# Kernel tuning notes

Hardware: AMD Instinct MI355X
Metric: run time of the kernel (lower is better)

## Reference

```python
import jax, jax.numpy as jnp
import numpy as np
from math import sqrt

NUM_HEADS = 16
NUM_KV_HEADS = 4
ROPE_BASE = 10000.0


def setup_inputs() -> dict:
    key = jax.random.key(0)
    ks = jax.random.split(key, 9)
    B, S, E = 4, 2048, 2048
    KV_DIM = NUM_KV_HEADS * (E // NUM_HEADS)  # 512
    s = 0.02
    return {
        "x": jax.random.normal(ks[0], (B, S, E), jnp.float32),
        "wq": jax.random.normal(ks[1], (E, E), jnp.float32) * s,
        "bq": jnp.zeros((E,), jnp.float32),
        "wk": jax.random.normal(ks[2], (KV_DIM, E), jnp.float32) * s,
        "bk": jnp.zeros((KV_DIM,), jnp.float32),
        "wv": jax.random.normal(ks[3], (KV_DIM, E), jnp.float32) * s,
        "bv": jnp.zeros((KV_DIM,), jnp.float32),
        "wo": jax.random.normal(ks[4], (E, E), jnp.float32) * s,
        "bo": jnp.zeros((E,), jnp.float32),
    }


def _rope_cos_sin(seq_len, head_dim, dtype):
    inv_freq = 1.0 / (ROPE_BASE ** (jnp.arange(0, head_dim, 2, dtype=jnp.float32) / head_dim))
    pos = jnp.arange(seq_len, dtype=jnp.float32)
    freqs = pos[:, None] * inv_freq[None, :]            # [S, D/2]
    emb = jnp.concatenate([freqs, freqs], axis=-1)      # [S, D]
    return jnp.cos(emb).astype(dtype), jnp.sin(emb).astype(dtype)


def _apply_rope(t, cos, sin):
    # t: [B, H, S, D]; cos/sin: [S, D]
    d2 = t.shape[-1] // 2
    rot = jnp.concatenate([-t[..., d2:], t[..., :d2]], axis=-1)
    return t * cos[None, None, :, :] + rot * sin[None, None, :, :]


def reference(x, wq, bq, wk, bk, wv, bv, wo, bo):
    B, S, E = x.shape
    H, KV = NUM_HEADS, NUM_KV_HEADS
    D = E // H
    G = H // KV

    q = (x @ wq.T + bq).reshape(B, S, H, D).transpose(0, 2, 1, 3)   # [B,H,S,D]
    k = (x @ wk.T + bk).reshape(B, S, KV, D).transpose(0, 2, 1, 3)  # [B,KV,S,D]
    v = (x @ wv.T + bv).reshape(B, S, KV, D).transpose(0, 2, 1, 3)

    cos, sin = _rope_cos_sin(S, D, x.dtype)
    q = _apply_rope(q, cos, sin)
    k = _apply_rope(k, cos, sin)

    # GQA: expand each kv head group_size times (contiguous repeat)
    k = jnp.repeat(k, G, axis=1)  # [B,H,S,D]
    v = jnp.repeat(v, G, axis=1)

    scores = jnp.einsum("bhqd,bhkd->bhqk", q, k)
    causal = jnp.triu(jnp.ones((S, S), dtype=bool), k=1)
    scores = jnp.where(causal[None, None, :, :], -jnp.inf, scores)
    attn = jax.nn.softmax(scores / sqrt(D), axis=-1)
    out = jnp.einsum("bhqk,bhkd->bhqd", attn, v)        # [B,H,S,D]
    out = out.transpose(0, 2, 1, 3).reshape(B, S, E)
    return out @ wo.T + bo
```

## Files before the change

### kernel.cpp

```cpp
#include <hip/hip_runtime.h>
#include <stdint.h>
#include <math.h>

typedef __attribute__((ext_vector_type(8))) short s16x8;
typedef __attribute__((ext_vector_type(4))) short s16x4;
typedef __attribute__((ext_vector_type(4))) float f32x4;

#define NEGH (-1.0e30f)

__device__ __forceinline__ short f2bf(float f) {
  union { float f; unsigned int i; } c; c.f = f;
  unsigned int lsb = (c.i >> 16) & 1u;
  c.i += 0x7fffu + lsb;
  return (short)(c.i >> 16);
}
__device__ __forceinline__ float bf2f(short u) {
  union { unsigned int i; float f; } c;
  c.i = ((unsigned int)(unsigned short)u) << 16;
  return c.f;
}

#define GLOAD_LDS16(gp, lp)                                                  \
  __builtin_amdgcn_global_load_lds(                                          \
      (__attribute__((address_space(1))) void*)(void*)(gp),                  \
      (__attribute__((address_space(3))) void*)(lp), 16, 0, 0)

__global__ __launch_bounds__(256) void cvt_kernel(const float* __restrict__ in,
                                                  short* __restrict__ out)
{
  const size_t i = ((size_t)blockIdx.x * 256 + threadIdx.x) * 4;
  const float4 v = *(const float4*)(in + i);
  s16x4 o = { f2bf(v.x), f2bf(v.y), f2bf(v.z), f2bf(v.w) };
  *(s16x4*)(out + i) = o;
}

__global__ __launch_bounds__(256) void gemm_bt(
    const short* __restrict__ A, const short* __restrict__ W,
    const float* __restrict__ bias, const float* __restrict__ bias2,
    void* __restrict__ C, void* __restrict__ C2,
    int M, int N, int K, int omode)
{
  __shared__ __align__(16) short As[128 * 64];
  __shared__ __align__(16) short Bs[128 * 64];

  const int t = threadIdx.x;
  const int l = t & 63;
  const int w = t >> 6;
  const int lane16 = l & 15;
  const int quad = l >> 4;
  const int wm = w >> 1, wn = w & 1;

  int bx = blockIdx.x, by = blockIdx.y;
  if (gridDim.x == 8 && gridDim.y == 64) {
    const int lid = blockIdx.x + 8 * blockIdx.y;
    const int xcd = lid & 7, idx = lid >> 3;
    by = xcd * 8 + (idx >> 3);
    bx = idx & 7;
  }
  const int mb0 = by * 128;
  const int nb0 = bx * 128;

  const f32x4 zero = {0.f, 0.f, 0.f, 0.f};
  f32x4 acc[4][4];
#pragma unroll
  for (int i = 0; i < 4; ++i)
#pragma unroll
    for (int j = 0; j < 4; ++j) acc[i][j] = zero;

  const int sr = t >> 3;
  const int sp = t & 7;
  const short* Ag = A + (size_t)(mb0 + sr) * K + sp * 8;
  const short* Wg = W + (size_t)(nb0 + sr) * K + sp * 8;
  short* Al = As + t * 8;
  short* Bl = Bs + t * 8;

  const int nkt = K >> 6;
  for (int kt = 0; kt < nkt; ++kt) {
    __syncthreads();
    const int kof = kt * 64;
#pragma unroll
    for (int it = 0; it < 4; ++it) {
      GLOAD_LDS16(Ag + kof + (size_t)(it * 32) * K, Al + it * 2048);
      GLOAD_LDS16(Wg + kof + (size_t)(it * 32) * K, Bl + it * 2048);
    }
    __syncthreads();
#pragma unroll
    for (int kk = 0; kk < 2; ++kk) {
      s16x8 af[4], bf[4];
#pragma unroll
      for (int mi = 0; mi < 4; ++mi)
        af[mi] = *(const s16x8*)&As[(wm * 64 + mi * 16 + lane16) * 64 +
                                    kk * 32 + quad * 8];
#pragma unroll
      for (int ni = 0; ni < 4; ++ni)
        bf[ni] = *(const s16x8*)&Bs[(wn * 64 + ni * 16 + lane16) * 64 +
                                    kk * 32 + quad * 8];
#pragma unroll
      for (int mi = 0; mi < 4; ++mi)
#pragma unroll
        for (int ni = 0; ni < 4; ++ni)
          acc[mi][ni] = __builtin_amdgcn_mfma_f32_16x16x32_bf16(
              af[mi], bf[ni], acc[mi][ni], 0, 0, 0);
    }
  }

#pragma unroll
  for (int ni = 0; ni < 4; ++ni) {
    const int n = nb0 + wn * 64 + ni * 16 + lane16;
    const float bvx = (omode == 3 && n >= 512) ? bias2[n - 512] : bias[n];
#pragma unroll
    for (int mi = 0; mi < 4; ++mi) {
      const int m0 = mb0 + wm * 64 + mi * 16 + quad * 4;
#pragma unroll
      for (int r = 0; r < 4; ++r) {
        const int m = m0 + r;
        const float v = acc[mi][ni][r] + bvx;
        if (omode == 0) {
          ((short*)C)[(size_t)m * N + n] = f2bf(v);
        } else if (omode == 1) {
          ((float*)C)[(size_t)m * N + n] = v;
        } else {
          if (n < 512) ((short*)C)[(size_t)m * 512 + n] = f2bf(v);
          else         ((short*)C2)[(size_t)m * 512 + (n - 512)] = f2bf(v);
        }
      }
    }
  }
}

__global__ __launch_bounds__(512, 2) void gemm256_bt(
    const short* __restrict__ A, const short* __restrict__ W,
    const float* __restrict__ bias, void* __restrict__ C,
    int M, int N, int K, int omode)
{
  __shared__ __align__(16) short Asm[2 * 16384];
  __shared__ __align__(16) short Bsm[2 * 16384];

  const int t = threadIdx.x;
  const int l = t & 63;
  const int w = t >> 6;
  const int lane16 = l & 15;
  const int quad = l >> 4;
  const int wm = w >> 2;
  const int wn = w & 3;

  int bx = blockIdx.x, by = blockIdx.y;
  if (gridDim.x == 8 && gridDim.y == 32) {
    const int bid = blockIdx.y * 8 + blockIdx.x;
    const int xcd = bid & 7, idx = bid >> 3;
    const int xc = xcd & 3, yc = xcd >> 2;
    bx = xc * 2 + (idx & 1);
    by = yc * 16 + (idx >> 1);
  }
  const int mb0 = by * 256;
  const int nb0 = bx * 256;

  const f32x4 zero = {0.f, 0.f, 0.f, 0.f};
  f32x4 acc[8][4];
#pragma unroll
  for (int i = 0; i < 8; ++i)
#pragma unroll
    for (int j = 0; j < 4; ++j) acc[i][j] = zero;

  const int srow = t >> 2;
  const int scs = (t & 3) ^ ((t >> 3) & 3);
  const short* Ag = A + (size_t)(mb0 + srow) * K + scs * 8;
  const short* Wg = W + (size_t)(nb0 + srow) * K + scs * 8;
  const size_t rstep = (size_t)128 * K;

#define STAGE_A(b, kt, kh)                                                    \
  do {                                                                        \
    const size_t ko_ = (size_t)(kt) * 64 + (kh) * 32;                         \
    GLOAD_LDS16(Ag + ko_,         Asm + (b) * 16384 + (kh) * 8192 + t * 8);   \
    GLOAD_LDS16(Ag + ko_ + rstep, Asm + (b) * 16384 + (kh) * 8192 + 4096 + t * 8); \
  } while (0)
#define STAGE_B(b, kt, kh)                                                    \
  do {                                                                        \
    const size_t ko_ = (size_t)(kt) * 64 + (kh) * 32;                         \
    GLOAD_LDS16(Wg + ko_,         Bsm + (b) * 16384 + (kh) * 8192 + t * 8);   \
    GLOAD_LDS16(Wg + ko_ + rstep, Bsm + (b) * 16384 + (kh) * 8192 + 4096 + t * 8); \
  } while (0)

  s16x8 bfr[4];

#define DO_PHASE(BUF, KK, MG, READB, STAGE_STMT, DO_VM)                       \
  {                                                                           \
    const short* Abase = Asm + (BUF) * 16384 + (KK) * 8192;                   \
    const short* Bbase = Bsm + (BUF) * 16384 + (KK) * 8192;                   \
    if (READB) {                                                              \
      _Pragma("unroll")                                                       \
      for (int ni = 0; ni < 4; ++ni) {                                        \
        const int nr = wn * 64 + ni * 16 + lane16;                            \
        bfr[ni] = *(const s16x8*)(Bbase + nr * 32 +                           \
                                  ((quad ^ ((nr >> 1) & 3)) << 3));           \
      }                                                                       \
    }                                                                         \
    s16x8 afr[4];                                                             \
    _Pragma("unroll")                                                         \
    for (int mi2 = 0; mi2 < 4; ++mi2) {                                       \
      const int mr = wm * 128 + (MG) * 64 + mi2 * 16 + lane16;                \
      afr[mi2] = *(const s16x8*)(Abase + mr * 32 +                            \
                                 ((quad ^ ((mr >> 1) & 3)) << 3));            \
    }                                                                         \
    STAGE_STMT;                                                               \
    __builtin_amdgcn_s_barrier();                                             \
    asm volatile("s_waitcnt lgkmcnt(0)" ::: "memory");                        \
    __builtin_amdgcn_sched_barrier(0);                                        \
    __builtin_amdgcn_s_setprio(1);                                            \
    _Pragma("unroll")                                                         \
    for (int mi2 = 0; mi2 < 4; ++mi2)                                         \
      _Pragma("unroll")                                                       \
      for (int ni = 0; ni < 4; ++ni)                                          \
        acc[(MG) * 4 + mi2][ni] = __builtin_amdgcn_mfma_f32_16x16x32_bf16(    \
            afr[mi2], bfr[ni], acc[(MG) * 4 + mi2][ni], 0, 0, 0);             \
    __builtin_amdgcn_s_setprio(0);                                            \
    if (DO_VM) {                                                              \
      asm volatile("s_waitcnt vmcnt(10)" ::: "memory");                       \
      __builtin_amdgcn_sched_barrier(0);                                      \
    }                                                                         \
    __builtin_amdgcn_s_barrier();                                             \
  }

  const int NT = K >> 6;

  STAGE_B(0, 0, 0); STAGE_A(0, 0, 0); STAGE_B(0, 0, 1); STAGE_A(0, 0, 1);
  STAGE_B(1, 1, 0); STAGE_A(1, 1, 0); STAGE_B(1, 1, 1);
  asm volatile("s_waitcnt vmcnt(10)" ::: "memory");
  __builtin_amdgcn_sched_barrier(0);
  __builtin_amdgcn_s_barrier();

  for (int i2 = 0; i2 < NT; i2 += 2) {
    const int tp1 = (i2 + 1 < NT) ? i2 + 1 : NT - 1;
    const int tp2 = (i2 + 2 < NT) ? i2 + 2 : NT - 1;
    const int tp3 = (i2 + 3 < NT) ? i2 + 3 : NT - 1;
    DO_PHASE(0, 0, 0, true,  STAGE_A(1, tp1, 1), false)
    DO_PHASE(0, 0, 1, false, STAGE_B(0, tp2, 0), true)
    DO_PHASE(0, 1, 0, true,  STAGE_A(0, tp2, 0), false)
    DO_PHASE(0, 1, 1, false, STAGE_B(0, tp2, 1), true)
    DO_PHASE(1, 0, 0, true,  STAGE_A(0, tp2, 1), false)
    DO_PHASE(1, 0, 1, false, STAGE_B(1, tp3, 0), true)
    DO_PHASE(1, 1, 0, true,  STAGE_A(1, tp3, 0), false)
    DO_PHASE(1, 1, 1, false, STAGE_B(1, tp3, 1), true)
  }

#pragma unroll
  for (int ni = 0; ni < 4; ++ni) {
    const int n = nb0 + wn * 64 + ni * 16 + lane16;
    const float bv = bias[n];
#pragma unroll
    for (int mi = 0; mi < 8; ++mi) {
      const int m0 = mb0 + wm * 128 + mi * 16 + quad * 4;
#pragma unroll
      for (int r = 0; r < 4; ++r) {
        const float v = acc[mi][ni][r] + bv;
        if (omode == 0) ((short*)C)[(size_t)(m0 + r) * N + n] = f2bf(v);
        else            ((float*)C)[(size_t)(m0 + r) * N + n] = v;
      }
    }
  }
#undef DO_PHASE
#undef STAGE_A
#undef STAGE_B
}

__global__ __launch_bounds__(256) void rope_tab_kernel(float2* __restrict__ tab)
{
  const int i = blockIdx.x * 256 + threadIdx.x;
  const int pos = i >> 6, d = i & 63;
  const float fr = (float)pos * exp2f((float)d * -0.20762050593048584f);
  float sn, cs;
  sincosf(fr, &sn, &cs);
  tab[i] = make_float2(cs, sn);
}

__global__ __launch_bounds__(256) void rope_kernel(short* __restrict__ buf,
                                                   int lognh,
                                                   const float2* __restrict__ tab)
{
  const int idx = blockIdx.x * 256 + threadIdx.x;
  const int d = idx & 63;
  const int rest = idx >> 6;
  const int row = rest >> lognh;
  const int pos = row & 2047;
  const float2 cssn = tab[(pos << 6) | d];
  const float cs = cssn.x, sn = cssn.y;
  const size_t base = (size_t)rest * 128 + d;
  const float lo = bf2f(buf[base]);
  const float hi = bf2f(buf[base + 64]);
  buf[base]      = f2bf(lo * cs - hi * sn);
  buf[base + 64] = f2bf(hi * cs + lo * sn);
}

__global__ __launch_bounds__(256) void trans_kernel(const short* __restrict__ in,
                                                    short* __restrict__ out)
{
  __shared__ short T[64 * 72];
  const int t = threadIdx.x;
  const int ms = blockIdx.x * 64;
  const int ns = blockIdx.y * 64;
  const int b = ms >> 11;
  const int sl = ms & 2047;
  const int r = t >> 3, sg = t & 7;
#pragma unroll
  for (int j = 0; j < 2; ++j) {
    const uint4 v = *(const uint4*)(in + (size_t)(ms + r + 32 * j) * 512 + ns + sg * 8);
    *(uint4*)&T[(r + 32 * j) * 72 + sg * 8] = v;
  }
  __syncthreads();
#pragma unroll
  for (int j = 0; j < 2; ++j) {
    const int nr = r + 32 * j;
    s16x8 v;
#pragma unroll
    for (int i = 0; i < 8; ++i) v[i] = T[(sg * 8 + i) * 72 + nr];
    *(s16x8*)(out + ((size_t)(b * 512 + ns + nr)) * 2048 + sl + sg * 8) = v;
  }
}

__global__ __launch_bounds__(512, 4) void attn_kernel(
    const short* __restrict__ qg, const short* __restrict__ kg,
    const short* __restrict__ vtg, short* __restrict__ og,
    const float2* __restrict__ tab)
{
  __shared__ __align__(16) short Ksm[2 * 64 * 128];
  __shared__ __align__(16) short Vsm[2 * 128 * 64];
  __shared__ __align__(16) short Psm[128 * 64];

  const int t = threadIdx.x;
  const int l = t & 63;
  const int w = t >> 6;
  const int lane16 = l & 15;
  const int quad = l >> 4;

  const int lid = blockIdx.x + 8 * (blockIdx.y + 16 * blockIdx.z);
  const int xcd = lid & 7, idx = lid >> 3;
  const int g = xcd * 2 + (idx >> 5);
  const int wv_ = idx & 31;
  const int b = g >> 2, kv = g & 3;
  const int h = kv * 4 + (wv_ >> 3);
  const int jb = wv_ & 7;

  const int krow = t >> 4, kseg = t & 15;
  const int vrow = t >> 3, vseg = t & 7;
  const int kswz = (kseg ^ (krow & 7)) * 8;
  const int vswz = (vseg ^ (vrow & 7)) * 8;

  const short* kbaseptr = kg + ((size_t)(b * 2048)) * 512 + kv * 128;
  const short* vbaseptr = vtg + ((size_t)(b * 512 + kv * 128)) * 2048;

  const float SC = 0.08838834764831845f * 1.4426950408889634f;
  const f32x4 zero = {0.f, 0.f, 0.f, 0.f};
  const int swz = (lane16 & 7) << 3;

  uint4 kr0, kr1, vr0, vr1;
#define LOADT(KB)                                                             \
  do {                                                                        \
    kr0 = *(const uint4*)(kbaseptr + (size_t)((KB) + krow) * 512 + kseg * 8); \
    kr1 = *(const uint4*)(kbaseptr + (size_t)((KB) + 32 + krow) * 512 + kseg * 8); \
    vr0 = *(const uint4*)(vbaseptr + (size_t)(vrow) * 2048 + (KB) + vseg * 8);     \
    vr1 = *(const uint4*)(vbaseptr + (size_t)(64 + vrow) * 2048 + (KB) + vseg * 8);\
  } while (0)
#define WRITET(c)                                                             \
  do {                                                                        \
    *(uint4*)&Ksm[(c) * 8192 + krow * 128 + kswz] = kr0;                      \
    *(uint4*)&Ksm[(c) * 8192 + (32 + krow) * 128 + kswz] = kr1;               \
    *(uint4*)&Vsm[(c) * 8192 + vrow * 64 + vswz] = vr0;                       \
    *(uint4*)&Vsm[(c) * 8192 + (64 + vrow) * 64 + vswz] = vr1;                \
  } while (0)

  for (int sp2 = 0; sp2 < 2; ++sp2) {
    const int jj = sp2 ? (15 - jb) : jb;
    const int qb0 = jj * 128;
    const int qw0 = qb0 + w * 16;
    const int qmaxw = qw0 + 15;
    const int ntl = 2 * jj + 2;

    s16x8 qf[4];
    {
      const short* qrow =
          qg + ((size_t)(b * 2048 + qw0 + lane16)) * 2048 + h * 128 + quad * 8;
      s16x8 qr[4];
#pragma unroll
      for (int kk = 0; kk < 4; ++kk) qr[kk] = *(const s16x8*)(qrow + kk * 32);
      const float2* tb = tab + (((size_t)(qw0 + lane16)) << 6) + quad * 8;
#pragma unroll
      for (int kk = 0; kk < 2; ++kk) {
        float lo[8], hi[8];
#pragma unroll
        for (int j = 0; j < 8; ++j) {
          const float2 cs2 = tb[kk * 32 + j];
          const float l0 = bf2f(qr[kk][j]);
          const float h0 = bf2f(qr[kk + 2][j]);
          lo[j] = l0 * cs2.x - h0 * cs2.y;
          hi[j] = h0 * cs2.x + l0 * cs2.y;
        }
        union { unsigned int u[4]; s16x8 v; } plo, phi;
#pragma unroll
        for (int j = 0; j < 4; ++j) {
          asm("v_cvt_pk_bf16_f32 %0, %1, %2"
              : "=v"(plo.u[j]) : "v"(lo[2 * j]), "v"(lo[2 * j + 1]));
          asm("v_cvt_pk_bf16_f32 %0, %1, %2"
              : "=v"(phi.u[j]) : "v"(hi[2 * j]), "v"(hi[2 * j + 1]));
        }
        qf[kk] = plo.v;
        qf[kk + 2] = phi.v;
      }
    }

    f32x4 o[8];
#pragma unroll
    for (int i = 0; i < 8; ++i) o[i] = zero;
    float m_i = NEGH, l_i = 0.f;

    LOADT(0);
    WRITET(0);
    __syncthreads();
    int cur = 0;

    for (int tl = 0; tl < ntl; ++tl) {
      const int kbase = tl * 64;
      if (tl + 1 < ntl) LOADT((tl + 1) * 64);

      if (kbase <= qmaxw) {
        const short* Kb = Ksm + cur * 8192;
        const short* Vb = Vsm + cur * 8192;
        f32x4 st[4];
#pragma unroll
        for (int mt = 0; mt < 4; ++mt) st[mt] = zero;
        __builtin_amdgcn_s_setprio(1);
#pragma unroll
        for (int mt = 0; mt < 4; ++mt) {
          const int rb = (mt * 16 + lane16) * 128;
#pragma unroll
          for (int kk = 0; kk < 4; ++kk) {
            const s16x8 a = *(const s16x8*)&Kb[rb + ((kk * 32 + quad * 8) ^ swz)];
            st[mt] = __builtin_amdgcn_mfma_f32_16x16x32_bf16(a, qf[kk], st[mt], 0, 0, 0);
          }
        }
        __builtin_amdgcn_s_setprio(0);

        const bool maskt = (kbase + 63 > qw0);
        const int qabs = qw0 + lane16;
        float tl_ = NEGH;
        if (maskt) {
#pragma unroll
          for (int mt = 0; mt < 4; ++mt)
#pragma unroll
            for (int r = 0; r < 4; ++r) {
              float xx = st[mt][r];
              if ((kbase + mt * 16 + quad * 4 + r) > qabs) xx = NEGH;
              st[mt][r] = xx;
              tl_ = fmaxf(tl_, xx);
            }
        } else {
#pragma unroll
          for (int mt = 0; mt < 4; ++mt)
#pragma unroll
            for (int r = 0; r < 4; ++r) tl_ = fmaxf(tl_, st[mt][r]);
        }
        tl_ = fmaxf(tl_, __shfl_xor(tl_, 16));
        tl_ = fmaxf(tl_, __shfl_xor(tl_, 32));
        const float mnew = fmaxf(m_i, tl_);
        if (!__all(tl_ <= m_i)) {
          const float alpha = exp2f((m_i - mnew) * SC);
          l_i *= alpha;
#pragma unroll
          for (int r = 0; r < 4; ++r) {
            const float ar = __shfl(alpha, quad * 4 + r);
#pragma unroll
            for (int ntd = 0; ntd < 8; ++ntd) o[ntd][r] *= ar;
          }
        }
        m_i = mnew;
        const float mS = mnew * SC;
        float rs = 0.f;
#pragma unroll
        for (int mt = 0; mt < 4; ++mt) {
          const float p0 = exp2f(fmaf(st[mt][0], SC, -mS));
          const float p1 = exp2f(fmaf(st[mt][1], SC, -mS));
          const float p2 = exp2f(fmaf(st[mt][2], SC, -mS));
          const float p3 = exp2f(fmaf(st[mt][3], SC, -mS));
          rs += (p0 + p1) + (p2 + p3);
          uint2 pk2;
          asm("v_cvt_pk_bf16_f32 %0, %1, %2" : "=v"(pk2.x) : "v"(p0), "v"(p1));
          asm("v_cvt_pk_bf16_f32 %0, %1, %2" : "=v"(pk2.y) : "v"(p2), "v"(p3));
          *(uint2*)&Psm[(w * 16 + lane16) * 64 + ((mt * 16 + quad * 4) ^ swz)] = pk2;
        }
        rs += __shfl_xor(rs, 16);
        rs += __shfl_xor(rs, 32);
        l_i += rs;

        const int prb = (w * 16 + lane16) * 64;
        __builtin_amdgcn_s_setprio(1);
#pragma unroll
        for (int kk = 0; kk < 2; ++kk) {
          const s16x8 pf = *(const s16x8*)&Psm[prb + ((kk * 32 + quad * 8) ^ swz)];
#pragma unroll
          for (int ntd = 0; ntd < 8; ++ntd) {
            const s16x8 vf =
                *(const s16x8*)&Vb[(ntd * 16 + lane16) * 64 + ((kk * 32 + quad * 8) ^ swz)];
            o[ntd] = __builtin_amdgcn_mfma_f32_16x16x32_bf16(pf, vf, o[ntd], 0, 0, 0);
          }
        }
        __builtin_amdgcn_s_setprio(0);
      }

      if (tl + 1 < ntl) WRITET(cur ^ 1);
      __syncthreads();
      cur ^= 1;
    }

#pragma unroll
    for (int r = 0; r < 4; ++r) {
      const float lr = __shfl(l_i, quad * 4 + r);
      const float inv = 1.f / lr;
      const size_t base =
          ((size_t)(b * 2048 + qw0 + quad * 4 + r)) * 2048 + h * 128 + lane16;
#pragma unroll
      for (int ntd = 0; ntd < 8; ++ntd) og[base + ntd * 16] = f2bf(o[ntd][r] * inv);
    }
  }
#undef LOADT
#undef WRITET
}

extern "C" void kernel_launch(void* const* d_in, const int* in_sizes, int n_in,
                              void* d_out, int out_size, void* d_ws,
                              size_t ws_size, hipStream_t stream)
{
  const float* x  = (const float*)d_in[0];
  const float* wq = (const float*)d_in[1];
  const float* bq = (const float*)d_in[2];
  const float* wk = (const float*)d_in[3];
  const float* bk = (const float*)d_in[4];
  const float* wv = (const float*)d_in[5];
  const float* bv = (const float*)d_in[6];
  const float* wo = (const float*)d_in[7];
  const float* bo = (const float*)d_in[8];
  float* out = (float*)d_out;

  char* ws = (char*)d_ws;
  short* xb  = (short*)ws;
  short* wqb = (short*)(ws + (32ull << 20));
  short* wkb = (short*)(ws + (40ull << 20));
  short* wvb = (short*)(ws + (42ull << 20));
  short* qws = (short*)(ws + (44ull << 20));
  float2* tab = (float2*)(ws + (76ull << 20));
  short* wob = xb;
  short* kws = (short*)d_out;
  short* vtw = (short*)((char*)d_out + (8ull << 20));
  short* vtmp = (short*)((char*)d_out + (16ull << 20));

  const dim3 blk(256);
  cvt_kernel<<<16384, blk, 0, stream>>>(x,  xb);
  cvt_kernel<<<4096,  blk, 0, stream>>>(wq, wqb);
  cvt_kernel<<<1024,  blk, 0, stream>>>(wk, wkb);
  cvt_kernel<<<1024,  blk, 0, stream>>>(wv, wvb);
  rope_tab_kernel<<<512, blk, 0, stream>>>(tab);
  gemm256_bt<<<dim3(8, 32), dim3(512), 0, stream>>>(xb, wqb, bq, qws, 8192, 2048, 2048, 0);
  gemm_bt<<<dim3(8, 64), blk, 0, stream>>>(xb, wkb, bk, bv, kws, vtmp, 8192, 1024, 2048, 3);
  trans_kernel<<<dim3(128, 8), blk, 0, stream>>>(vtmp, vtw);
  rope_kernel<<<8192, blk, 0, stream>>>(kws, 2, tab);
  cvt_kernel<<<4096, blk, 0, stream>>>(wo, wob);
  attn_kernel<<<dim3(8, 16, 4), dim3(512), 0, stream>>>(qws, kws, vtw, qws, tab);
  gemm256_bt<<<dim3(8, 32), dim3(512), 0, stream>>>(qws, wob, bo, out, 8192, 2048, 2048, 1);
}
```

Baseline: 504.9 us.

## Fuse weight conversions with rope table, relax gemm waits, streamline attention loads

Merges the three weight fp32-to-bf16 conversions and the rope table generation into one launch, which removes several small kernel launches. In the 256-thread gemm pipeline, the vmcnt waits drop from every other phase at vmcnt(10) to every fourth phase at vmcnt(6). The attention kernel now advances K/V load pointers incrementally instead of recomputing addresses each tile. Its row max is also computed as a tree reduction after masking rather than a serial chain. The wait change alters how many loads stay in flight, which could expose latency or affect correctness margins if counts are off.

```diff
diff --git a/kernel.cpp b/kernel.cpp
--- a/kernel.cpp
+++ b/kernel.cpp
@@ -32,6 +32,32 @@
   const float4 v = *(const float4*)(in + i);
   s16x4 o = { f2bf(v.x), f2bf(v.y), f2bf(v.z), f2bf(v.w) };
   *(s16x4*)(out + i) = o;
+}
+
+__global__ __launch_bounds__(256) void wcvt_kernel(
+    const float* __restrict__ wq, const float* __restrict__ wk,
+    const float* __restrict__ wv, short* __restrict__ wqb,
+    short* __restrict__ wkb, short* __restrict__ wvb,
+    float2* __restrict__ tab)
+{
+  const int bid = blockIdx.x;
+  if (bid < 6144) {
+    const float* in; short* out; int lb;
+    if (bid < 4096)      { in = wq; out = wqb; lb = bid; }
+    else if (bid < 5120) { in = wk; out = wkb; lb = bid - 4096; }
+    else                 { in = wv; out = wvb; lb = bid - 5120; }
+    const size_t i = ((size_t)lb * 256 + threadIdx.x) * 4;
+    const float4 v = *(const float4*)(in + i);
+    s16x4 o = { f2bf(v.x), f2bf(v.y), f2bf(v.z), f2bf(v.w) };
+    *(s16x4*)(out + i) = o;
+  } else {
+    const int i = (bid - 6144) * 256 + threadIdx.x;
+    const int d = i & 63;
+    const float fr = (float)(i >> 6) * exp2f((float)d * -0.20762050593048584f);
+    float sn, cs;
+    sincosf(fr, &sn, &cs);
+    tab[i] = make_float2(cs, sn);
+  }
 }
 
 __global__ __launch_bounds__(256) void gemm_bt(
@@ -181,9 +207,13 @@
     GLOAD_LDS16(Wg + ko_ + rstep, Bsm + (b) * 16384 + (kh) * 8192 + 4096 + t * 8); \
   } while (0)
 
+#define VMW6                                                                  \
+  asm volatile("s_waitcnt vmcnt(6)" ::: "memory");                            \
+  __builtin_amdgcn_sched_barrier(0);
+
   s16x8 bfr[4];
 
-#define DO_PHASE(BUF, KK, MG, READB, STAGE_STMT, DO_VM)                       \
+#define DO_PHASE(BUF, KK, MG, READB, STAGE_STMT, VM_STMT)                     \
   {                                                                           \
     const short* Abase = Asm + (BUF) * 16384 + (KK) * 8192;                   \
     const short* Bbase = Bsm + (BUF) * 16384 + (KK) * 8192;                   \
@@ -214,10 +244,7 @@
         acc[(MG) * 4 + mi2][ni] = __builtin_amdgcn_mfma_f32_16x16x32_bf16(    \
             afr[mi2], bfr[ni], acc[(MG) * 4 + mi2][ni], 0, 0, 0);             \
     __builtin_amdgcn_s_setprio(0);                                            \
-    if (DO_VM) {                                                              \
-      asm volatile("s_waitcnt vmcnt(10)" ::: "memory");                       \
-      __builtin_amdgcn_sched_barrier(0);                                      \
-    }                                                                         \
+    VM_STMT                                                                   \
     __builtin_amdgcn_s_barrier();                                             \
   }
 
@@ -225,7 +252,7 @@
 
   STAGE_B(0, 0, 0); STAGE_A(0, 0, 0); STAGE_B(0, 0, 1); STAGE_A(0, 0, 1);
   STAGE_B(1, 1, 0); STAGE_A(1, 1, 0); STAGE_B(1, 1, 1);
-  asm volatile("s_waitcnt vmcnt(10)" ::: "memory");
+  asm volatile("s_waitcnt vmcnt(6)" ::: "memory");
   __builtin_amdgcn_sched_barrier(0);
   __builtin_amdgcn_s_barrier();
 
@@ -233,14 +260,14 @@
     const int tp1 = (i2 + 1 < NT) ? i2 + 1 : NT - 1;
     const int tp2 = (i2 + 2 < NT) ? i2 + 2 : NT - 1;
     const int tp3 = (i2 + 3 < NT) ? i2 + 3 : NT - 1;
-    DO_PHASE(0, 0, 0, true,  STAGE_A(1, tp1, 1), false)
-    DO_PHASE(0, 0, 1, false, STAGE_B(0, tp2, 0), true)
-    DO_PHASE(0, 1, 0, true,  STAGE_A(0, tp2, 0), false)
-    DO_PHASE(0, 1, 1, false, STAGE_B(0, tp2, 1), true)
-    DO_PHASE(1, 0, 0, true,  STAGE_A(0, tp2, 1), false)
-    DO_PHASE(1, 0, 1, false, STAGE_B(1, tp3, 0), true)
-    DO_PHASE(1, 1, 0, true,  STAGE_A(1, tp3, 0), false)
-    DO_PHASE(1, 1, 1, false, STAGE_B(1, tp3, 1), true)
+    DO_PHASE(0, 0, 0, true,  STAGE_A(1, tp1, 1), )
+    DO_PHASE(0, 0, 1, false, STAGE_B(0, tp2, 0), )
+    DO_PHASE(0, 1, 0, true,  STAGE_A(0, tp2, 0), )
+    DO_PHASE(0, 1, 1, false, STAGE_B(0, tp2, 1), VMW6)
+    DO_PHASE(1, 0, 0, true,  STAGE_A(0, tp2, 1), )
+    DO_PHASE(1, 0, 1, false, STAGE_B(1, tp3, 0), )
+    DO_PHASE(1, 1, 0, true,  STAGE_A(1, tp3, 0), )
+    DO_PHASE(1, 1, 1, false, STAGE_B(1, tp3, 1), VMW6)
   }
 
 #pragma unroll
@@ -261,16 +288,7 @@
 #undef DO_PHASE
 #undef STAGE_A
 #undef STAGE_B
-}
-
-__global__ __launch_bounds__(256) void rope_tab_kernel(float2* __restrict__ tab)
-{
-  const int i = blockIdx.x * 256 + threadIdx.x;
-  const int pos = i >> 6, d = i & 63;
-  const float fr = (float)pos * exp2f((float)d * -0.20762050593048584f);
-  float sn, cs;
-  sincosf(fr, &sn, &cs);
-  tab[i] = make_float2(cs, sn);
+#undef VMW6
 }
 
 __global__ __launch_bounds__(256) void rope_kernel(short* __restrict__ buf,
@@ -353,12 +371,14 @@
   const int swz = (lane16 & 7) << 3;
 
   uint4 kr0, kr1, vr0, vr1;
-#define LOADT(KB)                                                             \
+#define LOADT()                                                               \
   do {                                                                        \
-    kr0 = *(const uint4*)(kbaseptr + (size_t)((KB) + krow) * 512 + kseg * 8); \
-    kr1 = *(const uint4*)(kbaseptr + (size_t)((KB) + 32 + krow) * 512 + kseg * 8); \
-    vr0 = *(const uint4*)(vbaseptr + (size_t)(vrow) * 2048 + (KB) + vseg * 8);     \
-    vr1 = *(const uint4*)(vbaseptr + (size_t)(64 + vrow) * 2048 + (KB) + vseg * 8);\
+    kr0 = *(const uint4*)kld;                                                 \
+    kr1 = *(const uint4*)(kld + 32 * 512);                                    \
+    vr0 = *(const uint4*)vld;                                                 \
+    vr1 = *(const uint4*)(vld + 64 * 2048);                                   \
+    kld += 64 * 512;                                                          \
+    vld += 64;                                                                \
   } while (0)
 #define WRITET(c)                                                             \
   do {                                                                        \
@@ -375,6 +395,9 @@
     const int qmaxw = qw0 + 15;
     const int ntl = 2 * jj + 2;
 
+    const short* kld = kbaseptr + (size_t)krow * 512 + kseg * 8;
+    const short* vld = vbaseptr + (size_t)vrow * 2048 + vseg * 8;
+
     s16x8 qf[4];
     {
       const short* qrow =
@@ -412,14 +435,14 @@
     for (int i = 0; i < 8; ++i) o[i] = zero;
     float m_i = NEGH, l_i = 0.f;
 
-    LOADT(0);
+    LOADT();
     WRITET(0);
     __syncthreads();
     int cur = 0;
 
     for (int tl = 0; tl < ntl; ++tl) {
       const int kbase = tl * 64;
-      if (tl + 1 < ntl) LOADT((tl + 1) * 64);
+      if (tl + 1 < ntl) LOADT();
 
       if (kbase <= qmaxw) {
         const short* Kb = Ksm + cur * 8192;
@@ -441,23 +464,20 @@
 
         const bool maskt = (kbase + 63 > qw0);
         const int qabs = qw0 + lane16;
-        float tl_ = NEGH;
         if (maskt) {
 #pragma unroll
           for (int mt = 0; mt < 4; ++mt)
 #pragma unroll
             for (int r = 0; r < 4; ++r) {
-              float xx = st[mt][r];
-              if ((kbase + mt * 16 + quad * 4 + r) > qabs) xx = NEGH;
-              st[mt][r] = xx;
-              tl_ = fmaxf(tl_, xx);
+              if ((kbase + mt * 16 + quad * 4 + r) > qabs) st[mt][r] = NEGH;
             }
-        } else {
-#pragma unroll
-          for (int mt = 0; mt < 4; ++mt)
-#pragma unroll
-            for (int r = 0; r < 4; ++r) tl_ = fmaxf(tl_, st[mt][r]);
-        }
+        }
+        float tm[4];
+#pragma unroll
+        for (int mt = 0; mt < 4; ++mt)
+          tm[mt] = fmaxf(fmaxf(st[mt][0], st[mt][1]),
+                         fmaxf(st[mt][2], st[mt][3]));
+        float tl_ = fmaxf(fmaxf(tm[0], tm[1]), fmaxf(tm[2], tm[3]));
         tl_ = fmaxf(tl_, __shfl_xor(tl_, 16));
         tl_ = fmaxf(tl_, __shfl_xor(tl_, 32));
         const float mnew = fmaxf(m_i, tl_);
@@ -552,11 +572,8 @@
   short* vtmp = (short*)((char*)d_out + (16ull << 20));
 
   const dim3 blk(256);
-  cvt_kernel<<<16384, blk, 0, stream>>>(x,  xb);
-  cvt_kernel<<<4096,  blk, 0, stream>>>(wq, wqb);
-  cvt_kernel<<<1024,  blk, 0, stream>>>(wk, wkb);
-  cvt_kernel<<<1024,  blk, 0, stream>>>(wv, wvb);
-  rope_tab_kernel<<<512, blk, 0, stream>>>(tab);
+  cvt_kernel<<<16384, blk, 0, stream>>>(x, xb);
+  wcvt_kernel<<<6656, blk, 0, stream>>>(wq, wkb == 0 ? 0 : wk, wv, wqb, wkb, wvb, tab);
   gemm256_bt<<<dim3(8, 32), dim3(512), 0, stream>>>(xb, wqb, bq, qws, 8192, 2048, 2048, 0);
   gemm_bt<<<dim3(8, 64), blk, 0, stream>>>(xb, wkb, bk, bv, kws, vtmp, 8192, 1024, 2048, 3);
   trans_kernel<<<dim3(128, 8), blk, 0, stream>>>(vtmp, vtw);
```

Result: faster. 492.8 us (-2.4%).
